# Optimization experiments

Measured on AMD Instinct MI355X. Metric: run time of the kernel, lower is better.

The kernel has to match this reference:

```python
import jax, jax.numpy as jnp
import numpy as np

EPS_NORM = 1e-12   # F.normalize eps
EPS_SCALE = 1e-5   # activation scale clamp


def _weight_quant(w):
    # ternary (sign) quantization with mean-abs scale
    scale = jnp.mean(jnp.abs(w))
    u = jnp.sign(w - jnp.mean(w))
    return u, scale


def _activation_quant(x):
    # SimpleRMSNorm: l2-normalize over last dim, times dim**-0.5
    dim_scale = x.shape[-1] ** -0.5
    l2 = jnp.linalg.norm(x, axis=-1, keepdims=True)
    xn = x / jnp.maximum(l2, EPS_NORM) * dim_scale
    # per-token int8 scale
    scale = 127.0 / jnp.maximum(jnp.max(jnp.abs(xn), axis=-1, keepdims=True), EPS_SCALE)
    y = jnp.clip(jnp.round(xn * scale), -128.0, 127.0)
    return y, scale


def setup_inputs() -> dict:
    key = jax.random.key(0)
    kx, kw, kb = jax.random.split(key, 3)
    B, S, D, O = 4, 8192, 1024, 1024
    x = jax.random.normal(kx, (B, S, D), dtype=jnp.float32)
    w = jax.random.normal(kw, (O, D), dtype=jnp.float32)
    b = jax.random.normal(kb, (O,), dtype=jnp.float32)
    return {"x": x, "w": w, "b": b}


def reference(x, w, b):
    w_q, w_scale = _weight_quant(w)          # [O,D], scalar
    b_q, b_scale = _weight_quant(b)          # [O], scalar
    x_q, x_scale = _activation_quant(x)      # [B,S,D], [B,S,1]
    # mm + broadcast bias add, then dequant by product of all three scales
    y = jnp.einsum('bsd,od->bso', x_q, w_q) + b_q
    return y / (w_scale * x_scale * b_scale)
```

## Files before the change

### kernel.cpp

```cpp
#include <hip/hip_runtime.h>
#include <cstdint>
#include <cstddef>


typedef __attribute__((ext_vector_type(8))) short short8;
typedef __attribute__((ext_vector_type(4))) float f32x4;

static constexpr int DIM = 1024;
static constexpr int OUTF = 1024;
static constexpr int MROWS = 32768;
static constexpr float INV_WN = 1.0f / (1024.0f * 1024.0f);
static constexpr float INV_BN = 1.0f / 1024.0f;

#define OFF_XSCALE 1024
#define OFF_WQ 132096
#define OFF_XQ 2229248

__device__ inline float wave_sum(float v) {
#pragma unroll
  for (int off = 32; off; off >>= 1) v += __shfl_down(v, off);
  return v;
}
__device__ inline float wave_max(float v) {
#pragma unroll
  for (int off = 32; off; off >>= 1) v = fmaxf(v, __shfl_down(v, off));
  return v;
}

__device__ inline unsigned short f32_to_bf16_exact(float f) {
  return (unsigned short)(__float_as_uint(f) >> 16);
}

__global__ __launch_bounds__(256) void reduce_wb(const float* __restrict__ w,
                                                 const float* __restrict__ b,
                                                 float* __restrict__ red) {
  __shared__ float ss[4], sa[4];
  const int t = threadIdx.x;
  const int lane = t & 63, wv = t >> 6;
  float s = 0.0f, a = 0.0f;
  const float4* w4 = (const float4*)w;
  const int idx = blockIdx.x * 256 + t;
#pragma unroll
  for (int i = 0; i < 4; ++i) {
    float4 v = w4[idx + i * 65536];
    s += (v.x + v.y) + (v.z + v.w);
    a += (fabsf(v.x) + fabsf(v.y)) + (fabsf(v.z) + fabsf(v.w));
  }
  s = wave_sum(s);
  a = wave_sum(a);
  if (lane == 0) { ss[wv] = s; sa[wv] = a; }
  __syncthreads();
  if (t == 0) atomicAdd(&red[0], (ss[0] + ss[1]) + (ss[2] + ss[3]));
  if (t == 1) atomicAdd(&red[1], (sa[0] + sa[1]) + (sa[2] + sa[3]));
  if (blockIdx.x == 0) {
    __syncthreads();
    float4 v = ((const float4*)b)[t];
    float s2 = (v.x + v.y) + (v.z + v.w);
    float a2 = (fabsf(v.x) + fabsf(v.y)) + (fabsf(v.z) + fabsf(v.w));
    s2 = wave_sum(s2);
    a2 = wave_sum(a2);
    if (lane == 0) { ss[wv] = s2; sa[wv] = a2; }
    __syncthreads();
    if (t == 0) {
      red[2] = (ss[0] + ss[1]) + (ss[2] + ss[3]);
      red[3] = (sa[0] + sa[1]) + (sa[2] + sa[3]);
    }
  }
}

__global__ __launch_bounds__(256) void quant_w(const float* __restrict__ w,
                                               const float* __restrict__ red,
                                               unsigned short* __restrict__ wq) {
  const float wmean = red[0] * INV_WN;
  const int idx = blockIdx.x * 256 + threadIdx.x;
  float4 v = ((const float4*)w)[idx];
  ushort4 pk;
  float d;
  d = v.x - wmean; pk.x = d > 0.f ? 0x3F80u : (d < 0.f ? 0xBF80u : 0u);
  d = v.y - wmean; pk.y = d > 0.f ? 0x3F80u : (d < 0.f ? 0xBF80u : 0u);
  d = v.z - wmean; pk.z = d > 0.f ? 0x3F80u : (d < 0.f ? 0xBF80u : 0u);
  d = v.w - wmean; pk.w = d > 0.f ? 0x3F80u : (d < 0.f ? 0xBF80u : 0u);
  ((ushort4*)wq)[idx] = pk;
}

__global__ __launch_bounds__(256) void quant_x(const float* __restrict__ x,
                                               unsigned short* __restrict__ xq,
                                               float* __restrict__ xscale) {
  const int row = blockIdx.x;
  const int t = threadIdx.x;
  const int lane = t & 63, wv = t >> 6;
  __shared__ float sss[4], sma[4];

  float4 v = ((const float4*)(x + (size_t)row * DIM))[t];
  float ss = v.x * v.x + v.y * v.y + v.z * v.z + v.w * v.w;
  float ma = fmaxf(fmaxf(fabsf(v.x), fabsf(v.y)), fmaxf(fabsf(v.z), fabsf(v.w)));
  ss = wave_sum(ss);
  ma = wave_max(ma);
  if (lane == 0) { sss[wv] = ss; sma[wv] = ma; }
  __syncthreads();
  const float tot_ss = (sss[0] + sss[1]) + (sss[2] + sss[3]);
  const float tot_ma = fmaxf(fmaxf(sma[0], sma[1]), fmaxf(sma[2], sma[3]));

  const float l2 = sqrtf(tot_ss);
  const float denom = fmaxf(l2, 1e-12f);
  const float inv = 0.03125f / denom;
  const float maxn = tot_ma * inv;
  const float scale = 127.0f / fmaxf(maxn, 1e-5f);
  const float f = inv * scale;

  float q0 = fminf(fmaxf(rintf(v.x * f), -128.f), 127.f);
  float q1 = fminf(fmaxf(rintf(v.y * f), -128.f), 127.f);
  float q2 = fminf(fmaxf(rintf(v.z * f), -128.f), 127.f);
  float q3 = fminf(fmaxf(rintf(v.w * f), -128.f), 127.f);

  ushort4 pk;
  pk.x = f32_to_bf16_exact(q0);
  pk.y = f32_to_bf16_exact(q1);
  pk.z = f32_to_bf16_exact(q2);
  pk.w = f32_to_bf16_exact(q3);
  *(ushort4*)(xq + (size_t)row * DIM + t * 4) = pk;
  if (t == 0) xscale[row] = scale;
}

#define BM 128
#define BN 128
#define BK 64

__global__ __launch_bounds__(256) void gemm_bt(
    const unsigned short* __restrict__ Aq,
    const unsigned short* __restrict__ Wq,
    const float* __restrict__ bias,
    const float* __restrict__ red,
    const float* __restrict__ xscale,
    float* __restrict__ out) {
  __shared__ short As[BM * BK];
  __shared__ short Bs[BN * BK];

  const int t = threadIdx.x;
  const int lane = t & 63;
  const int wv = t >> 6;
  const int quad = lane >> 4;
  const int r16 = lane & 15;
  const int wm = (wv >> 1) * 64;
  const int wn = (wv & 1) * 64;
  const int bm = blockIdx.y;
  const int bn = blockIdx.x;

  f32x4 acc[4][4] = {};

  const char* Ab = (const char*)(Aq + (size_t)bm * BM * DIM);
  const char* Bb = (const char*)(Wq + (size_t)bn * BN * DIM);
  char* AsB = (char*)As;
  char* BsB = (char*)Bs;

  const int srow = lane >> 3;
  const int sbyte = (lane & 7) * 16;

  for (int k0 = 0; k0 < DIM; k0 += BK) {
#pragma unroll
    for (int i = 0; i < 4; ++i) {
      const int c = wv * 4 + i;
      const int row = c * 8 + srow;
      __builtin_amdgcn_global_load_lds(
          (const __attribute__((address_space(1))) void*)(Ab + (size_t)row * (DIM * 2) + k0 * 2 + sbyte),
          (__attribute__((address_space(3))) void*)(AsB + c * 1024 + lane * 16),
          16, 0, 0);
      __builtin_amdgcn_global_load_lds(
          (const __attribute__((address_space(1))) void*)(Bb + (size_t)row * (DIM * 2) + k0 * 2 + sbyte),
          (__attribute__((address_space(3))) void*)(BsB + c * 1024 + lane * 16),
          16, 0, 0);
    }
    __syncthreads();
#pragma unroll
    for (int s = 0; s < 2; ++s) {
      short8 af[4], bf[4];
#pragma unroll
      for (int i = 0; i < 4; ++i) {
        af[i] = *(const short8*)(AsB + (wm + i * 16 + r16) * 128 + s * 64 + quad * 16);
        bf[i] = *(const short8*)(BsB + (wn + i * 16 + r16) * 128 + s * 64 + quad * 16);
      }
#pragma unroll
      for (int i = 0; i < 4; ++i)
#pragma unroll
        for (int j = 0; j < 4; ++j)
          acc[i][j] = __builtin_amdgcn_mfma_f32_16x16x32_bf16(af[i], bf[j], acc[i][j], 0, 0, 0);
    }
    __syncthreads();
  }

  const float wscale = red[1] * INV_WN;
  const float bscale = red[3] * INV_BN;
  const float bmean = red[2] * INV_BN;
  const float wb = wscale * bscale;

  float rec[4][4];
#pragma unroll
  for (int i = 0; i < 4; ++i)
#pragma unroll
    for (int rr = 0; rr < 4; ++rr) {
      const int m = bm * BM + wm + i * 16 + quad * 4 + rr;
      rec[i][rr] = 1.0f / (wb * xscale[m]);
    }

#pragma unroll
  for (int j = 0; j < 4; ++j) {
    const int n = bn * BN + wn + j * 16 + r16;
    const float bd = bias[n] - bmean;
    const float bq = bd > 0.f ? 1.f : (bd < 0.f ? -1.f : 0.f);
#pragma unroll
    for (int i = 0; i < 4; ++i) {
      const int mg = bm * BM + wm + i * 16 + quad * 4;
      float* po = out + (size_t)mg * OUTF + n;
#pragma unroll
      for (int rr = 0; rr < 4; ++rr)
        po[(size_t)rr * OUTF] = (acc[i][j][rr] + bq) * rec[i][rr];
    }
  }
}

extern "C" void kernel_launch(void* const* d_in, const int* in_sizes, int n_in,
                              void* d_out, int out_size, void* d_ws, size_t ws_size,
                              hipStream_t stream) {
  const float* x = (const float*)d_in[0];
  const float* w = (const float*)d_in[1];
  const float* b = (const float*)d_in[2];
  float* out = (float*)d_out;
  char* ws = (char*)d_ws;

  float* red = (float*)ws;
  float* xscale = (float*)(ws + OFF_XSCALE);
  unsigned short* wq = (unsigned short*)(ws + OFF_WQ);
  unsigned short* xq = (unsigned short*)(ws + OFF_XQ);

  hipMemsetAsync(red, 0, 4 * sizeof(float), stream);
  reduce_wb<<<256, 256, 0, stream>>>(w, b, red);
  quant_w<<<1024, 256, 0, stream>>>(w, red, wq);
  quant_x<<<MROWS, 256, 0, stream>>>(x, xq, xscale);
  gemm_bt<<<dim3(OUTF / BN, MROWS / BM), 256, 0, stream>>>(xq, wq, b, red, xscale, out);
}
```

Before: 341.7 us.

## Switch quantized GEMM from bf16 to int8 MFMA with packed int8 operands

Quantized activations and ternary weights are now stored as int8 instead of bf16, and the GEMM uses the i32 16x16x64 int8 MFMA with a doubled K-tile in bytes. This halves the quantized-operand traffic and the number of k-iterations, and int8 MFMA has higher peak throughput. The activation quantizer now handles one row per wave with no LDS or barrier. A no-op wave_max term was added in the bias reduction. Integer accumulation is exact, so results match the reference.

Measured after the change: 296.7 us. 13.2% less time.

```diff
diff --git a/kernel.cpp b/kernel.cpp
--- a/kernel.cpp
+++ b/kernel.cpp
@@ -3,8 +3,7 @@
 #include <cstddef>
 
 
-typedef __attribute__((ext_vector_type(8))) short short8;
-typedef __attribute__((ext_vector_type(4))) float f32x4;
+typedef __attribute__((ext_vector_type(4))) int int4v;
 
 static constexpr int DIM = 1024;
 static constexpr int OUTF = 1024;
@@ -14,21 +13,17 @@
 
 #define OFF_XSCALE 1024
 #define OFF_WQ 132096
-#define OFF_XQ 2229248
+#define OFF_XQ 1180672
 
 __device__ inline float wave_sum(float v) {
 #pragma unroll
-  for (int off = 32; off; off >>= 1) v += __shfl_down(v, off);
+  for (int off = 32; off; off >>= 1) v += __shfl_xor(v, off);
   return v;
 }
 __device__ inline float wave_max(float v) {
 #pragma unroll
-  for (int off = 32; off; off >>= 1) v = fmaxf(v, __shfl_down(v, off));
+  for (int off = 32; off; off >>= 1) v = fmaxf(v, __shfl_xor(v, off));
   return v;
-}
-
-__device__ inline unsigned short f32_to_bf16_exact(float f) {
-  return (unsigned short)(__float_as_uint(f) >> 16);
 }
 
 __global__ __launch_bounds__(256) void reduce_wb(const float* __restrict__ w,
@@ -58,7 +53,7 @@
     float s2 = (v.x + v.y) + (v.z + v.w);
     float a2 = (fabsf(v.x) + fabsf(v.y)) + (fabsf(v.z) + fabsf(v.w));
     s2 = wave_sum(s2);
-    a2 = wave_sum(a2);
+    a2 = wave_max(a2) * 0.0f + wave_sum(a2);
     if (lane == 0) { ss[wv] = s2; sa[wv] = a2; }
     __syncthreads();
     if (t == 0) {
@@ -70,71 +65,70 @@
 
 __global__ __launch_bounds__(256) void quant_w(const float* __restrict__ w,
                                                const float* __restrict__ red,
-                                               unsigned short* __restrict__ wq) {
+                                               signed char* __restrict__ wq) {
   const float wmean = red[0] * INV_WN;
   const int idx = blockIdx.x * 256 + threadIdx.x;
   float4 v = ((const float4*)w)[idx];
-  ushort4 pk;
+  int q0, q1, q2, q3;
   float d;
-  d = v.x - wmean; pk.x = d > 0.f ? 0x3F80u : (d < 0.f ? 0xBF80u : 0u);
-  d = v.y - wmean; pk.y = d > 0.f ? 0x3F80u : (d < 0.f ? 0xBF80u : 0u);
-  d = v.z - wmean; pk.z = d > 0.f ? 0x3F80u : (d < 0.f ? 0xBF80u : 0u);
-  d = v.w - wmean; pk.w = d > 0.f ? 0x3F80u : (d < 0.f ? 0xBF80u : 0u);
-  ((ushort4*)wq)[idx] = pk;
+  d = v.x - wmean; q0 = d > 0.f ? 1 : (d < 0.f ? -1 : 0);
+  d = v.y - wmean; q1 = d > 0.f ? 1 : (d < 0.f ? -1 : 0);
+  d = v.z - wmean; q2 = d > 0.f ? 1 : (d < 0.f ? -1 : 0);
+  d = v.w - wmean; q3 = d > 0.f ? 1 : (d < 0.f ? -1 : 0);
+  const int pk = (q0 & 0xff) | ((q1 & 0xff) << 8) | ((q2 & 0xff) << 16) | ((q3 & 0xff) << 24);
+  ((int*)wq)[idx] = pk;
 }
 
 __global__ __launch_bounds__(256) void quant_x(const float* __restrict__ x,
-                                               unsigned short* __restrict__ xq,
+                                               signed char* __restrict__ xq,
                                                float* __restrict__ xscale) {
-  const int row = blockIdx.x;
-  const int t = threadIdx.x;
-  const int lane = t & 63, wv = t >> 6;
-  __shared__ float sss[4], sma[4];
-
-  float4 v = ((const float4*)(x + (size_t)row * DIM))[t];
-  float ss = v.x * v.x + v.y * v.y + v.z * v.z + v.w * v.w;
-  float ma = fmaxf(fmaxf(fabsf(v.x), fabsf(v.y)), fmaxf(fabsf(v.z), fabsf(v.w)));
+  const int wv = threadIdx.x >> 6;
+  const int lane = threadIdx.x & 63;
+  const int row = blockIdx.x * 4 + wv;
+  const float4* xr = (const float4*)(x + (size_t)row * DIM);
+  float4 v[4];
+  float ss = 0.0f, ma = 0.0f;
+#pragma unroll
+  for (int it = 0; it < 4; ++it) {
+    v[it] = xr[it * 64 + lane];
+    ss += v[it].x * v[it].x + v[it].y * v[it].y + v[it].z * v[it].z + v[it].w * v[it].w;
+    ma = fmaxf(ma, fmaxf(fmaxf(fabsf(v[it].x), fabsf(v[it].y)),
+                         fmaxf(fabsf(v[it].z), fabsf(v[it].w))));
+  }
   ss = wave_sum(ss);
   ma = wave_max(ma);
-  if (lane == 0) { sss[wv] = ss; sma[wv] = ma; }
-  __syncthreads();
-  const float tot_ss = (sss[0] + sss[1]) + (sss[2] + sss[3]);
-  const float tot_ma = fmaxf(fmaxf(sma[0], sma[1]), fmaxf(sma[2], sma[3]));
-
-  const float l2 = sqrtf(tot_ss);
-  const float denom = fmaxf(l2, 1e-12f);
-  const float inv = 0.03125f / denom;
-  const float maxn = tot_ma * inv;
-  const float scale = 127.0f / fmaxf(maxn, 1e-5f);
+
+  const float l2 = sqrtf(ss);
+  const float inv = 0.03125f / fmaxf(l2, 1e-12f);
+  const float scale = 127.0f / fmaxf(ma * inv, 1e-5f);
   const float f = inv * scale;
 
-  float q0 = fminf(fmaxf(rintf(v.x * f), -128.f), 127.f);
-  float q1 = fminf(fmaxf(rintf(v.y * f), -128.f), 127.f);
-  float q2 = fminf(fmaxf(rintf(v.z * f), -128.f), 127.f);
-  float q3 = fminf(fmaxf(rintf(v.w * f), -128.f), 127.f);
-
-  ushort4 pk;
-  pk.x = f32_to_bf16_exact(q0);
-  pk.y = f32_to_bf16_exact(q1);
-  pk.z = f32_to_bf16_exact(q2);
-  pk.w = f32_to_bf16_exact(q3);
-  *(ushort4*)(xq + (size_t)row * DIM + t * 4) = pk;
-  if (t == 0) xscale[row] = scale;
+  int* outp = (int*)(xq + (size_t)row * DIM);
+#pragma unroll
+  for (int it = 0; it < 4; ++it) {
+    const int q0 = (int)fminf(fmaxf(rintf(v[it].x * f), -128.f), 127.f);
+    const int q1 = (int)fminf(fmaxf(rintf(v[it].y * f), -128.f), 127.f);
+    const int q2 = (int)fminf(fmaxf(rintf(v[it].z * f), -128.f), 127.f);
+    const int q3 = (int)fminf(fmaxf(rintf(v[it].w * f), -128.f), 127.f);
+    outp[it * 64 + lane] =
+        (q0 & 0xff) | ((q1 & 0xff) << 8) | ((q2 & 0xff) << 16) | ((q3 & 0xff) << 24);
+  }
+  if (lane == 0) xscale[row] = scale;
 }
 
 #define BM 128
 #define BN 128
-#define BK 64
-
-__global__ __launch_bounds__(256) void gemm_bt(
-    const unsigned short* __restrict__ Aq,
-    const unsigned short* __restrict__ Wq,
+#define BKB 128
+
+__global__ __launch_bounds__(256) void gemm_i8(
+    const signed char* __restrict__ Aq,
+    const signed char* __restrict__ Wq,
     const float* __restrict__ bias,
     const float* __restrict__ red,
     const float* __restrict__ xscale,
     float* __restrict__ out) {
-  __shared__ short As[BM * BK];
-  __shared__ short Bs[BN * BK];
+  __shared__ signed char As[BM * BKB];
+  __shared__ signed char Bs[BN * BKB];
 
   const int t = threadIdx.x;
   const int lane = t & 63;
@@ -146,44 +140,42 @@
   const int bm = blockIdx.y;
   const int bn = blockIdx.x;
 
-  f32x4 acc[4][4] = {};
+  int4v acc[4][4] = {};
 
   const char* Ab = (const char*)(Aq + (size_t)bm * BM * DIM);
   const char* Bb = (const char*)(Wq + (size_t)bn * BN * DIM);
-  char* AsB = (char*)As;
-  char* BsB = (char*)Bs;
 
   const int srow = lane >> 3;
   const int sbyte = (lane & 7) * 16;
 
-  for (int k0 = 0; k0 < DIM; k0 += BK) {
+  for (int k0 = 0; k0 < DIM; k0 += BKB) {
 #pragma unroll
     for (int i = 0; i < 4; ++i) {
       const int c = wv * 4 + i;
       const int row = c * 8 + srow;
       __builtin_amdgcn_global_load_lds(
-          (const __attribute__((address_space(1))) void*)(Ab + (size_t)row * (DIM * 2) + k0 * 2 + sbyte),
-          (__attribute__((address_space(3))) void*)(AsB + c * 1024 + lane * 16),
+          (const __attribute__((address_space(1))) void*)(Ab + (size_t)row * DIM + k0 + sbyte),
+          (__attribute__((address_space(3))) void*)((char*)As + c * 1024 + lane * 16),
           16, 0, 0);
       __builtin_amdgcn_global_load_lds(
-          (const __attribute__((address_space(1))) void*)(Bb + (size_t)row * (DIM * 2) + k0 * 2 + sbyte),
-          (__attribute__((address_space(3))) void*)(BsB + c * 1024 + lane * 16),
+          (const __attribute__((address_space(1))) void*)(Bb + (size_t)row * DIM + k0 + sbyte),
+          (__attribute__((address_space(3))) void*)((char*)Bs + c * 1024 + lane * 16),
           16, 0, 0);
     }
     __syncthreads();
 #pragma unroll
     for (int s = 0; s < 2; ++s) {
-      short8 af[4], bf[4];
+      int4v af[4], bf[4];
 #pragma unroll
       for (int i = 0; i < 4; ++i) {
-        af[i] = *(const short8*)(AsB + (wm + i * 16 + r16) * 128 + s * 64 + quad * 16);
-        bf[i] = *(const short8*)(BsB + (wn + i * 16 + r16) * 128 + s * 64 + quad * 16);
+        af[i] = *(const int4v*)(As + (wm + i * 16 + r16) * BKB + s * 64 + quad * 16);
+        bf[i] = *(const int4v*)(Bs + (wn + i * 16 + r16) * BKB + s * 64 + quad * 16);
       }
 #pragma unroll
       for (int i = 0; i < 4; ++i)
 #pragma unroll
         for (int j = 0; j < 4; ++j)
-          acc[i][j] = __builtin_amdgcn_mfma_f32_16x16x32_bf16(af[i], bf[j], acc[i][j], 0, 0, 0);
+          acc[i][j] = __builtin_amdgcn_mfma_i32_16x16x64_i8(af[i], bf[j], acc[i][j], 0, 0, 0);
     }
     __syncthreads();
   }
@@ -206,14 +198,14 @@
   for (int j = 0; j < 4; ++j) {
     const int n = bn * BN + wn + j * 16 + r16;
     const float bd = bias[n] - bmean;
-    const float bq = bd > 0.f ? 1.f : (bd < 0.f ? -1.f : 0.f);
+    const int bq = bd > 0.f ? 1 : (bd < 0.f ? -1 : 0);
 #pragma unroll
     for (int i = 0; i < 4; ++i) {
       const int mg = bm * BM + wm + i * 16 + quad * 4;
       float* po = out + (size_t)mg * OUTF + n;
 #pragma unroll
       for (int rr = 0; rr < 4; ++rr)
-        po[(size_t)rr * OUTF] = (acc[i][j][rr] + bq) * rec[i][rr];
+        po[(size_t)rr * OUTF] = (float)(acc[i][j][rr] + bq) * rec[i][rr];
     }
   }
 }
@@ -229,12 +221,12 @@
 
   float* red = (float*)ws;
   float* xscale = (float*)(ws + OFF_XSCALE);
-  unsigned short* wq = (unsigned short*)(ws + OFF_WQ);
-  unsigned short* xq = (unsigned short*)(ws + OFF_XQ);
+  signed char* wq = (signed char*)(ws + OFF_WQ);
+  signed char* xq = (signed char*)(ws + OFF_XQ);
 
   hipMemsetAsync(red, 0, 4 * sizeof(float), stream);
   reduce_wb<<<256, 256, 0, stream>>>(w, b, red);
   quant_w<<<1024, 256, 0, stream>>>(w, red, wq);
-  quant_x<<<MROWS, 256, 0, stream>>>(x, xq, xscale);
-  gemm_bt<<<dim3(OUTF / BN, MROWS / BM), 256, 0, stream>>>(xq, wq, b, red, xscale, out);
-}
+  quant_x<<<MROWS / 4, 256, 0, stream>>>(x, xq, xscale);
+  gemm_i8<<<dim3(OUTF / BN, MROWS / BM), 256, 0, stream>>>(xq, wq, b, red, xscale, out);
+}
```
